# Optimization experiments

Measured on AMD Instinct MI355X. Metric: run time of the kernel, lower is better.

Reference implementation:

```python
import jax, jax.numpy as jnp
import numpy as np

B, T, D, H, K, TAU, L = 1024, 168, 32, 512, 8, 24, 2


def _cell(Wih, Whh, bih, bhh, x_t, h, c):
    # PyTorch LSTM gate order: i, f, g, o
    gates = x_t @ Wih.T + bih + h @ Whh.T + bhh  # [B, 4H]
    i, f, g, o = jnp.split(gates, 4, axis=-1)
    c = jax.nn.sigmoid(f) * c + jax.nn.sigmoid(i) * jnp.tanh(g)
    h = jax.nn.sigmoid(o) * jnp.tanh(c)
    return h, c


def setup_inputs() -> dict:
    key = jax.random.key(0)
    ks = jax.random.split(key, 22)
    s = 1.0 / np.sqrt(H)

    def u(k, shape):
        return jax.random.uniform(k, shape, jnp.float32, -s, s)

    inp = {"x": jax.random.normal(ks[0], (B, T, D), jnp.float32)}
    # encoder LSTM (layer0 input D, layer1 input H)
    inp["enc_Wih0"] = u(ks[1], (4 * H, D)); inp["enc_Whh0"] = u(ks[2], (4 * H, H))
    inp["enc_bih0"] = u(ks[3], (4 * H,));  inp["enc_bhh0"] = u(ks[4], (4 * H,))
    inp["enc_Wih1"] = u(ks[5], (4 * H, H)); inp["enc_Whh1"] = u(ks[6], (4 * H, H))
    inp["enc_bih1"] = u(ks[7], (4 * H,));  inp["enc_bhh1"] = u(ks[8], (4 * H,))
    # decoder LSTM (both layers input H since d_enopt == d_model)
    inp["dec_Wih0"] = u(ks[9], (4 * H, H));  inp["dec_Whh0"] = u(ks[10], (4 * H, H))
    inp["dec_bih0"] = u(ks[11], (4 * H,));   inp["dec_bhh0"] = u(ks[12], (4 * H,))
    inp["dec_Wih1"] = u(ks[13], (4 * H, H)); inp["dec_Whh1"] = u(ks[14], (4 * H, H))
    inp["dec_bih1"] = u(ks[15], (4 * H,));   inp["dec_bhh1"] = u(ks[16], (4 * H,))
    # output heads
    inp["W1"] = u(ks[17], (K, H)); inp["b1"] = u(ks[18], (K,))
    inp["W2"] = u(ks[19], (K, H)); inp["b2"] = u(ks[20], (K,))
    return inp


def reference(x, enc_Wih0, enc_Whh0, enc_bih0, enc_bhh0,
              enc_Wih1, enc_Whh1, enc_bih1, enc_bhh1,
              dec_Wih0, dec_Whh0, dec_bih0, dec_bhh0,
              dec_Wih1, dec_Whh1, dec_bih1, dec_bhh1,
              W1, b1, W2, b2):
    enc_params = [(enc_Wih0, enc_Whh0, enc_bih0, enc_bhh0),
                  (enc_Wih1, enc_Whh1, enc_bih1, enc_bhh1)]
    dec_params = [(dec_Wih0, dec_Whh0, dec_bih0, dec_bhh0),
                  (dec_Wih1, dec_Whh1, dec_bih1, dec_bhh1)]
    b = x.shape[0]
    h0 = jnp.zeros((L, b, H), x.dtype)
    c0 = jnp.zeros((L, b, H), x.dtype)

    def enc_step(carry, x_t):
        h, c = carry
        inp = x_t
        hs, cs = [], []
        for l, p in enumerate(enc_params):
            hn, cn = _cell(*p, inp, h[l], c[l])
            hs.append(hn); cs.append(cn); inp = hn
        return (jnp.stack(hs), jnp.stack(cs)), None

    (h, c), _ = jax.lax.scan(enc_step, (h0, c0), jnp.swapaxes(x, 0, 1))

    def dec_step(carry, _):
        h, c = carry
        inp = h[L - 1]  # feed top-layer hidden back as input
        hs, cs = [], []
        for l, p in enumerate(dec_params):
            hn, cn = _cell(*p, inp, h[l], c[l])
            hs.append(hn); cs.append(cn); inp = hn
        return (jnp.stack(hs), jnp.stack(cs)), inp  # top-layer output

    _, outs = jax.lax.scan(dec_step, (h, c), None, length=TAU)  # [TAU, B, H]
    out = jnp.swapaxes(outs, 0, 1)  # [B, TAU, H]
    mu = out @ W1.T + b1
    beta = 2.0
    sigma = jax.nn.softplus(beta * (out @ W2.T + b2)) / beta
    return mu, sigma
```

## Files before the change

### kernel.cpp

```cpp
#include <hip/hip_runtime.h>
#include <math.h>

typedef _Float16 f16;
typedef __attribute__((ext_vector_type(8))) _Float16 f16x8;
typedef __attribute__((ext_vector_type(4))) _Float16 f16x4;
typedef __attribute__((ext_vector_type(4))) float f32x4;

namespace {
constexpr int B_ = 1024, T_ = 168, H_ = 512, K_ = 8, TAU_ = 24, U_ = 192;
}

__device__ __forceinline__ float sig_(float x) { return 1.0f / (1.0f + expf(-x)); }

template<int AUX>
__device__ __forceinline__ void gl16(const f16* g, char* l) {
    __builtin_amdgcn_global_load_lds((const __attribute__((address_space(1))) void*)g,
                                     (__attribute__((address_space(3))) void*)l, 16, 0, AUX);
}
__device__ __forceinline__ void st_h_sc1(f16* p, f16 v) {
    unsigned int u = (unsigned int)__builtin_bit_cast(unsigned short, v);
    asm volatile("global_store_short %0, %1, off sc1" :: "v"(p), "v"(u) : "memory");
}
#define MFMA16 __builtin_amdgcn_mfma_f32_16x16x32_f16

struct PP {
    const f16 *xp, *w0p, *wsW;
    const float* bsum;
    const f16* hzero;
    f16 *h0r, *h1r;
    f16* h1dec;
    int *cnt0, *cnt1;
};

extern "C" __global__ void __launch_bounds__(256, 1)
lstm_persist(PP P)
{
    extern __shared__ char lds[];
    const int tid = threadIdx.x;
    const int id2 = (blockIdx.x & 7) * 32 + (blockIdx.x >> 3);
    const int rt  = id2 & 15;
    const int row0 = rt * 64;
    const int j0   = (id2 >> 4) * 32;

    const int lane = tid & 63, wid = tid >> 6;
    const int l16 = lane & 15, lq = lane >> 4;
    const int wr = wid >> 1, wc = wid & 1;
    const int sr = tid >> 3, sl = tid & 7;
    const long ksw = (long)((sl ^ (sr & 7)) << 3);

    long wgrow[4];
    #pragma unroll
    for (int q = 0; q < 4; ++q) {
        const int r = sr + 32 * q;
        wgrow[q] = (long)(((r >> 4) & 3) * H_ + j0 + ((r >> 6) << 4) + (r & 15));
    }
    const int swz = (l16 & 7) << 4;
    const int ab0 = (wr * 32 + l16) * 128;
    const int ab1 = ab0 + 2048;
    int wb[4];
    #pragma unroll
    for (int nf = 0; nf < 4; ++nf) wb[nf] = (wc * 64 + nf * 16 + l16) * 128;

    const size_t WM  = (size_t)2048 * 512;
    const long   NBH = (long)B_ * H_;
    bool dead = false;

    auto waitf = [&](const int* p) {
        if (tid == 0 && !dead) {
            int tries = 0;
            while (__hip_atomic_load(p, __ATOMIC_RELAXED,
                                     __HIP_MEMORY_SCOPE_AGENT) < 16) {
                __builtin_amdgcn_s_sleep(1);
                if (++tries > (1 << 16)) { dead = true; break; }
            }
        }
        __syncthreads();
    };
    auto signal = [&](int* p) {
        asm volatile("s_waitcnt vmcnt(0)" ::: "memory");
        __syncthreads();
        if (tid == 0)
            __hip_atomic_fetch_add(p, 1, __ATOMIC_RELAXED, __HIP_MEMORY_SCOPE_AGENT);
    };

    auto runCell = [&](const f16* Ain, long ldaIn, int ncIn, long KwIn,
                       const f16* Wih, const f16* Hin, const f16* Whh,
                       const float* bs, float* cst, f16* hout) {
        const long aA0 = (long)(row0 + sr) * ldaIn + ksw;
        const long aA1 = aA0 + 32 * ldaIn;
        const long aH0 = (long)(row0 + sr) * H_ + ksw;
        const long aH1 = aH0 + 32 * H_;
        const long wI0 = wgrow[0] * KwIn + ksw, wI1 = wgrow[1] * KwIn + ksw;
        const long wI2 = wgrow[2] * KwIn + ksw, wI3 = wgrow[3] * KwIn + ksw;
        const long wH0 = wgrow[0] * H_ + ksw, wH1 = wgrow[1] * H_ + ksw;
        const long wH2 = wgrow[2] * H_ + ksw, wH3 = wgrow[3] * H_ + ksw;
        const int NC = ncIn + 8;

        auto stageChunk = [&](int ci, int buf) {
            char* lb = lds + buf * 24576;
            if (ci < ncIn) {
                const long k0 = (long)ci << 6;
                gl16<16>(Ain + aA0 + k0, lb + tid * 16);
                gl16<16>(Ain + aA1 + k0, lb + 4096 + tid * 16);
                gl16<0>(Wih + wI0 + k0, lb + 8192  + tid * 16);
                gl16<0>(Wih + wI1 + k0, lb + 12288 + tid * 16);
                gl16<0>(Wih + wI2 + k0, lb + 16384 + tid * 16);
                gl16<0>(Wih + wI3 + k0, lb + 20480 + tid * 16);
            } else {
                const long k0 = (long)(ci - ncIn) << 6;
                gl16<16>(Hin + aH0 + k0, lb + tid * 16);
                gl16<16>(Hin + aH1 + k0, lb + 4096 + tid * 16);
                gl16<0>(Whh + wH0 + k0, lb + 8192  + tid * 16);
                gl16<0>(Whh + wH1 + k0, lb + 12288 + tid * 16);
                gl16<0>(Whh + wH2 + k0, lb + 16384 + tid * 16);
                gl16<0>(Whh + wH3 + k0, lb + 20480 + tid * 16);
            }
        };

        f32x4 acc[4][2];
        #pragma unroll
        for (int nf = 0; nf < 4; ++nf)
            #pragma unroll
            for (int m = 0; m < 2; ++m)
                #pragma unroll
                for (int q = 0; q < 4; ++q) acc[nf][m][q] = 0.f;

        stageChunk(0, 0); stageChunk(1, 1); stageChunk(2, 2);
        stageChunk(3, 3); stageChunk(4, 4);
        int cb = 0, sb = 5;
        for (int i = 0; i < NC; ++i) {
            const int ahead = (NC - 1 - i) < 4 ? (NC - 1 - i) : 4;
            if      (ahead == 4) asm volatile("s_waitcnt vmcnt(24)" ::: "memory");
            else if (ahead == 3) asm volatile("s_waitcnt vmcnt(18)" ::: "memory");
            else if (ahead == 2) asm volatile("s_waitcnt vmcnt(12)" ::: "memory");
            else if (ahead == 1) asm volatile("s_waitcnt vmcnt(6)"  ::: "memory");
            else                 asm volatile("s_waitcnt vmcnt(0)"  ::: "memory");
            __builtin_amdgcn_s_barrier();

            char* lb = lds + cb * 24576;
            #pragma unroll
            for (int ks = 0; ks < 2; ++ks) {
                const int kb = ((ks * 64) + lq * 16) ^ swz;
                f16x8 ah0 = *(const f16x8*)(lb + ab0 + kb);
                f16x8 ah1 = *(const f16x8*)(lb + ab1 + kb);
                #pragma unroll
                for (int nf = 0; nf < 4; ++nf) {
                    f16x8 wv = *(const f16x8*)(lb + 8192 + wb[nf] + kb);
                    acc[nf][0] = MFMA16(ah0, wv, acc[nf][0], 0, 0, 0);
                    acc[nf][1] = MFMA16(ah1, wv, acc[nf][1], 0, 0, 0);
                }
            }
            asm volatile("s_waitcnt lgkmcnt(0)" ::: "memory");
            __builtin_amdgcn_s_barrier();
            if (i + 5 < NC) { stageChunk(i + 5, sb); sb = (sb == 5) ? 0 : sb + 1; }
            cb = (cb == 5) ? 0 : cb + 1;
        }

        const int j = j0 + wc * 16 + l16;
        const float bg0 = bs[j], bg1 = bs[H_ + j];
        const float bg2 = bs[2 * H_ + j], bg3 = bs[3 * H_ + j];
        #pragma unroll
        for (int m = 0; m < 2; ++m)
            #pragma unroll
            for (int r = 0; r < 4; ++r) {
                const int ci = m * 4 + r;
                const int bb = row0 + wr * 32 + m * 16 + lq * 4 + r;
                const long base = (long)bb * H_ + j;
                const float pi = acc[0][m][r] + bg0;
                const float pf = acc[1][m][r] + bg1;
                const float pg = acc[2][m][r] + bg2;
                const float po = acc[3][m][r] + bg3;
                const float cn = sig_(pf) * cst[ci] + sig_(pi) * tanhf(pg);
                const float hn = sig_(po) * tanhf(cn);
                cst[ci] = cn;
                st_h_sc1(&hout[base], (f16)hn);
            }
    };

    float c0st[8], c1st[8];
    #pragma unroll
    for (int i = 0; i < 8; ++i) { c0st[i] = 0.f; c1st[i] = 0.f; }

    for (int u = 0; u < U_; ++u) {
        const bool dec = (u >= T_);
        const f16* h0prev = (u == 0) ? P.hzero : P.h0r + (long)((u - 1) & 7) * NBH;
        const f16* h1prev = (u == 0) ? P.hzero
                          : (u <= T_ ? P.h1r + (long)((u - 1) & 7) * NBH
                                     : P.h1dec + (long)(u - 1 - T_) * NBH);
        f16* h0out = P.h0r + (long)(u & 7) * NBH;

        if (dec) {
            waitf(P.cnt1 + (u - 1) * 16 + rt);
            runCell(h1prev, H_, 8, H_, P.wsW + 3 * WM, h0prev,
                    P.wsW + 4 * WM, P.bsum + 4096, c0st, h0out);
        } else {
            runCell(P.xp + (long)u * B_ * 64, 64, 1, 64, P.w0p, h0prev,
                    P.wsW, P.bsum, c0st, h0out);
        }
        signal(P.cnt0 + u * 16 + rt);

        waitf(P.cnt0 + u * 16 + rt);
        f16* h1out = (u < T_) ? P.h1r + (long)(u & 7) * NBH
                              : P.h1dec + (long)(u - T_) * NBH;
        runCell(h0out, H_, 8, H_,
                dec ? P.wsW + 5 * WM : P.wsW + 1 * WM, h1prev,
                dec ? P.wsW + 6 * WM : P.wsW + 2 * WM,
                P.bsum + (dec ? 6144 : 2048), c1st, h1out);
        signal(P.cnt1 + u * 16 + rt);
    }
}

extern "C" __global__ void __launch_bounds__(256)
padx_kernel(const float* __restrict__ x, f16* __restrict__ xp)
{
    const int idx = blockIdx.x * 256 + threadIdx.x;
    const int t = idx >> 10, b = idx & 1023;
    const float* src = x + ((long)b * T_ + t) * 32;
    f16* dst = xp + (long)idx * 64;
    #pragma unroll
    for (int q = 0; q < 8; ++q) {
        float4 v = *(const float4*)&src[q * 4];
        *(f16x4*)&dst[q * 4] = (f16x4){(f16)v.x, (f16)v.y, (f16)v.z, (f16)v.w};
    }
    #pragma unroll
    for (int q = 8; q < 16; ++q) *(f16x4*)&dst[q * 4] = (f16x4){0, 0, 0, 0};
}

extern "C" __global__ void __launch_bounds__(256)
padw_kernel(const float* __restrict__ w, f16* __restrict__ dst)
{
    const int idx = blockIdx.x * 256 + threadIdx.x;
    const int row = idx >> 4, k4 = idx & 15;
    f16x4 hv = (f16x4){0, 0, 0, 0};
    if (k4 < 8) {
        float4 v = *(const float4*)&w[(long)row * 32 + k4 * 4];
        hv = (f16x4){(f16)v.x, (f16)v.y, (f16)v.z, (f16)v.w};
    }
    *(f16x4*)&dst[(long)row * 64 + k4 * 4] = hv;
}

extern "C" __global__ void __launch_bounds__(256)
wcvt_kernel(const float* s0, const float* s1, const float* s2, const float* s3,
            const float* s4, const float* s5, const float* s6, f16* dst)
{
    const int i = blockIdx.x * 256 + threadIdx.x;
    if (i >= 7 * 262144) return;
    const int m = i >> 18, off = i & 262143;
    const float* s = m == 0 ? s0 : m == 1 ? s1 : m == 2 ? s2 : m == 3 ? s3
                   : m == 4 ? s4 : m == 5 ? s5 : s6;
    float4 v = ((const float4*)s)[off];
    *(f16x4*)&dst[(long)m * 1048576 + (long)off * 4] =
        (f16x4){(f16)v.x, (f16)v.y, (f16)v.z, (f16)v.w};
}

extern "C" __global__ void __launch_bounds__(256)
bias_kernel(const float* a0, const float* b0, const float* a1, const float* b1,
            const float* a2, const float* b2, const float* a3, const float* b3,
            float* out)
{
    const int i = blockIdx.x * 256 + threadIdx.x;
    const int l = i >> 11, k = i & 2047;
    const float* pa = l == 0 ? a0 : l == 1 ? a1 : l == 2 ? a2 : a3;
    const float* pb = l == 0 ? b0 : l == 1 ? b1 : l == 2 ? b2 : b3;
    out[i] = pa[k] + pb[k];
}

extern "C" __global__ void __launch_bounds__(256)
zero16(uint4* p, int n)
{
    for (int i = blockIdx.x * 256 + threadIdx.x; i < n; i += gridDim.x * 256)
        p[i] = make_uint4(0, 0, 0, 0);
}

extern "C" __global__ void __launch_bounds__(256)
head_all(const f16* __restrict__ h1dec,
         const float* __restrict__ W1, const float* __restrict__ b1,
         const float* __restrict__ W2, const float* __restrict__ b2,
         float* __restrict__ out)
{
    const int blk = blockIdx.x;
    const int s = blk >> 6;
    const int idx = (blk & 63) * 256 + threadIdx.x;
    const int b = idx >> 4, rr = idx & 15, k = rr & 7, which = rr >> 3;
    const float* w  = (which ? W2 : W1) + (long)k * H_;
    const f16*   hp = h1dec + ((long)s * B_ + b) * H_;
    float sum = 0.f;
    for (int d = 0; d < H_; d += 8) {
        f16x8  hv = *(const f16x8*)&hp[d];
        float4 w0 = *(const float4*)&w[d];
        float4 w1 = *(const float4*)&w[d + 4];
        sum = fmaf((float)hv[0], w0.x, sum);
        sum = fmaf((float)hv[1], w0.y, sum);
        sum = fmaf((float)hv[2], w0.z, sum);
        sum = fmaf((float)hv[3], w0.w, sum);
        sum = fmaf((float)hv[4], w1.x, sum);
        sum = fmaf((float)hv[5], w1.y, sum);
        sum = fmaf((float)hv[6], w1.z, sum);
        sum = fmaf((float)hv[7], w1.w, sum);
    }
    const long o = ((long)b * TAU_ + s) * K_ + k;
    if (which == 0) {
        out[o] = sum + b1[k];
    } else {
        float z  = 2.0f * (sum + b2[k]);
        float sp = fmaxf(z, 0.0f) + log1pf(expf(-fabsf(z)));
        out[(long)B_ * TAU_ * K_ + o] = 0.5f * sp;
    }
}

extern "C" void kernel_launch(void* const* d_in, const int* in_sizes, int n_in,
                              void* d_out, int out_size, void* d_ws, size_t ws_size,
                              hipStream_t stream)
{
    (void)in_sizes; (void)n_in; (void)out_size; (void)ws_size;

    const float* x     = (const float*)d_in[0];
    const float* eWih0 = (const float*)d_in[1];
    const float* eWhh0 = (const float*)d_in[2];
    const float* ebih0 = (const float*)d_in[3];
    const float* ebhh0 = (const float*)d_in[4];
    const float* eWih1 = (const float*)d_in[5];
    const float* eWhh1 = (const float*)d_in[6];
    const float* ebih1 = (const float*)d_in[7];
    const float* ebhh1 = (const float*)d_in[8];
    const float* dWih0 = (const float*)d_in[9];
    const float* dWhh0 = (const float*)d_in[10];
    const float* dbih0 = (const float*)d_in[11];
    const float* dbhh0 = (const float*)d_in[12];
    const float* dWih1 = (const float*)d_in[13];
    const float* dWhh1 = (const float*)d_in[14];
    const float* dbih1 = (const float*)d_in[15];
    const float* dbhh1 = (const float*)d_in[16];
    const float* W1    = (const float*)d_in[17];
    const float* b1    = (const float*)d_in[18];
    const float* W2    = (const float*)d_in[19];
    const float* b2    = (const float*)d_in[20];
    float* out = (float*)d_out;

    (void)hipFuncSetAttribute((const void*)lstm_persist,
                              hipFuncAttributeMaxDynamicSharedMemorySize, 147456);

    char* wsp = (char*)d_ws;
    auto take = [&](size_t n) { void* p = (void*)wsp; wsp += n; return p; };

    f16* xp    = (f16*)take((size_t)T_ * B_ * 64 * 2);
    f16* w0p   = (f16*)take((size_t)2048 * 64 * 2);
    f16* wsW   = (f16*)take((size_t)7 * 2048 * 512 * 2);
    float* bsum = (float*)take((size_t)4 * 2048 * 4);
    f16* h1dec = (f16*)take((size_t)TAU_ * B_ * H_ * 2);
    f16* h0r   = (f16*)take((size_t)8 * B_ * H_ * 2);
    f16* h1r   = (f16*)take((size_t)8 * B_ * H_ * 2);

    char* zstart = wsp;
    int* cnt0  = (int*)take((size_t)U_ * 16 * 4);
    int* cnt1  = (int*)take((size_t)U_ * 16 * 4);
    f16* hzero = (f16*)take((size_t)B_ * H_ * 2);
    const size_t zeroBytes = (size_t)(wsp - zstart);

    const dim3 blk(256);

    padx_kernel<<<dim3(T_ * B_ / 256), blk, 0, stream>>>(x, xp);
    padw_kernel<<<dim3(128), blk, 0, stream>>>(eWih0, w0p);
    wcvt_kernel<<<dim3(7168), blk, 0, stream>>>(eWhh0, eWih1, eWhh1, dWih0,
                                                dWhh0, dWih1, dWhh1, wsW);
    bias_kernel<<<dim3(32), blk, 0, stream>>>(ebih0, ebhh0, ebih1, ebhh1,
                                              dbih0, dbhh0, dbih1, dbhh1, bsum);
    zero16<<<dim3(256), blk, 0, stream>>>((uint4*)zstart, (int)(zeroBytes / 16));

    PP args;
    args.xp = xp; args.w0p = w0p; args.wsW = wsW; args.bsum = bsum; args.hzero = hzero;
    args.h0r = h0r; args.h1r = h1r; args.h1dec = h1dec;
    args.cnt0 = cnt0; args.cnt1 = cnt1;

    lstm_persist<<<dim3(256), blk, 147456, stream>>>(args);
    head_all<<<dim3(TAU_ * 64), blk, 0, stream>>>(h1dec, W1, b1, W2, b2, out);
}
```

Before: 5.247 ms.

## Wavefront-fuse encoder layer1 step s-1 with layer0 step s in one pipeline

During the encoder, layer-1 of step s-1 and layer-0 of step s now run inside one staged load/MFMA pipeline that shares the 6 LDS buffers. A single combined signal and wait per step replaces the two cross-block syncs per timestep. This targets the grid-wide synchronisation latency and the pipeline fill and drain at each cell boundary. The decoder keeps the sequential two-sync schedule, and a tail call finishes the last layer-1 step. It also issues the next stage before waiting, with prefetch depth 5, and drops the special cache hint on the x input loads. The cost is more complex dependency reasoning and an extra accumulator set, which adds register pressure.

```diff
diff --git a/kernel.cpp b/kernel.cpp
--- a/kernel.cpp
+++ b/kernel.cpp
@@ -64,6 +64,16 @@
     const size_t WM  = (size_t)2048 * 512;
     const long   NBH = (long)B_ * H_;
     bool dead = false;
+
+    struct Cd {
+        const f16 *Ain; long lda; int ncIn; long Kw;
+        const f16 *Wih, *Hin, *Whh;
+        const float* bg; float* cst; f16* hout; bool axc;
+    };
+
+    float c0st[8], c1st[8];
+    #pragma unroll
+    for (int i = 0; i < 8; ++i) { c0st[i] = 0.f; c1st[i] = 0.f; }
 
     auto waitf = [&](const int* p) {
         if (tid == 0 && !dead) {
@@ -76,89 +86,40 @@
         }
         __syncthreads();
     };
-    auto signal = [&](int* p) {
+    auto sig1 = [&](int* p) {
         asm volatile("s_waitcnt vmcnt(0)" ::: "memory");
         __syncthreads();
         if (tid == 0)
             __hip_atomic_fetch_add(p, 1, __ATOMIC_RELAXED, __HIP_MEMORY_SCOPE_AGENT);
     };
-
-    auto runCell = [&](const f16* Ain, long ldaIn, int ncIn, long KwIn,
-                       const f16* Wih, const f16* Hin, const f16* Whh,
-                       const float* bs, float* cst, f16* hout) {
-        const long aA0 = (long)(row0 + sr) * ldaIn + ksw;
-        const long aA1 = aA0 + 32 * ldaIn;
-        const long aH0 = (long)(row0 + sr) * H_ + ksw;
-        const long aH1 = aH0 + 32 * H_;
-        const long wI0 = wgrow[0] * KwIn + ksw, wI1 = wgrow[1] * KwIn + ksw;
-        const long wI2 = wgrow[2] * KwIn + ksw, wI3 = wgrow[3] * KwIn + ksw;
-        const long wH0 = wgrow[0] * H_ + ksw, wH1 = wgrow[1] * H_ + ksw;
-        const long wH2 = wgrow[2] * H_ + ksw, wH3 = wgrow[3] * H_ + ksw;
-        const int NC = ncIn + 8;
-
-        auto stageChunk = [&](int ci, int buf) {
-            char* lb = lds + buf * 24576;
-            if (ci < ncIn) {
-                const long k0 = (long)ci << 6;
-                gl16<16>(Ain + aA0 + k0, lb + tid * 16);
-                gl16<16>(Ain + aA1 + k0, lb + 4096 + tid * 16);
-                gl16<0>(Wih + wI0 + k0, lb + 8192  + tid * 16);
-                gl16<0>(Wih + wI1 + k0, lb + 12288 + tid * 16);
-                gl16<0>(Wih + wI2 + k0, lb + 16384 + tid * 16);
-                gl16<0>(Wih + wI3 + k0, lb + 20480 + tid * 16);
-            } else {
-                const long k0 = (long)(ci - ncIn) << 6;
-                gl16<16>(Hin + aH0 + k0, lb + tid * 16);
-                gl16<16>(Hin + aH1 + k0, lb + 4096 + tid * 16);
-                gl16<0>(Whh + wH0 + k0, lb + 8192  + tid * 16);
-                gl16<0>(Whh + wH1 + k0, lb + 12288 + tid * 16);
-                gl16<0>(Whh + wH2 + k0, lb + 16384 + tid * 16);
-                gl16<0>(Whh + wH3 + k0, lb + 20480 + tid * 16);
+    auto sig2 = [&](int* p, int* q) {
+        asm volatile("s_waitcnt vmcnt(0)" ::: "memory");
+        __syncthreads();
+        if (tid == 0) {
+            __hip_atomic_fetch_add(p, 1, __ATOMIC_RELAXED, __HIP_MEMORY_SCOPE_AGENT);
+            __hip_atomic_fetch_add(q, 1, __ATOMIC_RELAXED, __HIP_MEMORY_SCOPE_AGENT);
+        }
+    };
+
+    auto computeChunk = [&](char* lb, f32x4 (&acc)[4][2]) {
+        #pragma unroll
+        for (int ks = 0; ks < 2; ++ks) {
+            const int kb = ((ks * 64) + lq * 16) ^ swz;
+            f16x8 ah0 = *(const f16x8*)(lb + ab0 + kb);
+            f16x8 ah1 = *(const f16x8*)(lb + ab1 + kb);
+            #pragma unroll
+            for (int nf = 0; nf < 4; ++nf) {
+                f16x8 wv = *(const f16x8*)(lb + 8192 + wb[nf] + kb);
+                acc[nf][0] = MFMA16(ah0, wv, acc[nf][0], 0, 0, 0);
+                acc[nf][1] = MFMA16(ah1, wv, acc[nf][1], 0, 0, 0);
             }
-        };
-
-        f32x4 acc[4][2];
-        #pragma unroll
-        for (int nf = 0; nf < 4; ++nf)
-            #pragma unroll
-            for (int m = 0; m < 2; ++m)
-                #pragma unroll
-                for (int q = 0; q < 4; ++q) acc[nf][m][q] = 0.f;
-
-        stageChunk(0, 0); stageChunk(1, 1); stageChunk(2, 2);
-        stageChunk(3, 3); stageChunk(4, 4);
-        int cb = 0, sb = 5;
-        for (int i = 0; i < NC; ++i) {
-            const int ahead = (NC - 1 - i) < 4 ? (NC - 1 - i) : 4;
-            if      (ahead == 4) asm volatile("s_waitcnt vmcnt(24)" ::: "memory");
-            else if (ahead == 3) asm volatile("s_waitcnt vmcnt(18)" ::: "memory");
-            else if (ahead == 2) asm volatile("s_waitcnt vmcnt(12)" ::: "memory");
-            else if (ahead == 1) asm volatile("s_waitcnt vmcnt(6)"  ::: "memory");
-            else                 asm volatile("s_waitcnt vmcnt(0)"  ::: "memory");
-            __builtin_amdgcn_s_barrier();
-
-            char* lb = lds + cb * 24576;
-            #pragma unroll
-            for (int ks = 0; ks < 2; ++ks) {
-                const int kb = ((ks * 64) + lq * 16) ^ swz;
-                f16x8 ah0 = *(const f16x8*)(lb + ab0 + kb);
-                f16x8 ah1 = *(const f16x8*)(lb + ab1 + kb);
-                #pragma unroll
-                for (int nf = 0; nf < 4; ++nf) {
-                    f16x8 wv = *(const f16x8*)(lb + 8192 + wb[nf] + kb);
-                    acc[nf][0] = MFMA16(ah0, wv, acc[nf][0], 0, 0, 0);
-                    acc[nf][1] = MFMA16(ah1, wv, acc[nf][1], 0, 0, 0);
-                }
-            }
-            asm volatile("s_waitcnt lgkmcnt(0)" ::: "memory");
-            __builtin_amdgcn_s_barrier();
-            if (i + 5 < NC) { stageChunk(i + 5, sb); sb = (sb == 5) ? 0 : sb + 1; }
-            cb = (cb == 5) ? 0 : cb + 1;
         }
-
+    };
+
+    auto epi = [&](const Cd& c, f32x4 (&a)[4][2]) {
         const int j = j0 + wc * 16 + l16;
-        const float bg0 = bs[j], bg1 = bs[H_ + j];
-        const float bg2 = bs[2 * H_ + j], bg3 = bs[3 * H_ + j];
+        const float bg0 = c.bg[j], bg1 = c.bg[H_ + j];
+        const float bg2 = c.bg[2 * H_ + j], bg3 = c.bg[3 * H_ + j];
         #pragma unroll
         for (int m = 0; m < 2; ++m)
             #pragma unroll
@@ -166,47 +127,133 @@
                 const int ci = m * 4 + r;
                 const int bb = row0 + wr * 32 + m * 16 + lq * 4 + r;
                 const long base = (long)bb * H_ + j;
-                const float pi = acc[0][m][r] + bg0;
-                const float pf = acc[1][m][r] + bg1;
-                const float pg = acc[2][m][r] + bg2;
-                const float po = acc[3][m][r] + bg3;
-                const float cn = sig_(pf) * cst[ci] + sig_(pi) * tanhf(pg);
+                const float pi = a[0][m][r] + bg0;
+                const float pf = a[1][m][r] + bg1;
+                const float pg = a[2][m][r] + bg2;
+                const float po = a[3][m][r] + bg3;
+                const float cn = sig_(pf) * c.cst[ci] + sig_(pi) * tanhf(pg);
                 const float hn = sig_(po) * tanhf(cn);
-                cst[ci] = cn;
-                st_h_sc1(&hout[base], (f16)hn);
+                c.cst[ci] = cn;
+                st_h_sc1(&c.hout[base], (f16)hn);
             }
     };
 
-    float c0st[8], c1st[8];
-    #pragma unroll
-    for (int i = 0; i < 8; ++i) { c0st[i] = 0.f; c1st[i] = 0.f; }
-
-    for (int u = 0; u < U_; ++u) {
-        const bool dec = (u >= T_);
-        const f16* h0prev = (u == 0) ? P.hzero : P.h0r + (long)((u - 1) & 7) * NBH;
-        const f16* h1prev = (u == 0) ? P.hzero
-                          : (u <= T_ ? P.h1r + (long)((u - 1) & 7) * NBH
-                                     : P.h1dec + (long)(u - 1 - T_) * NBH);
-        f16* h0out = P.h0r + (long)(u & 7) * NBH;
-
+    auto runPipe = [&](const Cd& c1, const Cd& c0, bool two) {
+        const int NC1 = c1.ncIn + 8;
+        const int NT  = two ? NC1 + c0.ncIn + 8 : NC1;
+
+        auto stageG = [&](int g) {
+            const Cd& c = (g < NC1) ? c1 : c0;
+            const int ci = (g < NC1) ? g : g - NC1;
+            char* lb = lds + (g % 6) * 24576;
+            const f16 *Ap, *Wp; long lda, Kw, k0; bool axc;
+            if (ci < c.ncIn) { Ap = c.Ain; Wp = c.Wih; lda = c.lda; Kw = c.Kw;
+                               k0 = (long)ci << 6; axc = c.axc; }
+            else             { Ap = c.Hin; Wp = c.Whh; lda = H_; Kw = H_;
+                               k0 = (long)(ci - c.ncIn) << 6; axc = false; }
+            const long aB = (long)(row0 + sr) * lda + ksw + k0;
+            if (axc) {
+                gl16<0>(Ap + aB, lb + tid * 16);
+                gl16<0>(Ap + aB + 32 * lda, lb + 4096 + tid * 16);
+            } else {
+                gl16<16>(Ap + aB, lb + tid * 16);
+                gl16<16>(Ap + aB + 32 * lda, lb + 4096 + tid * 16);
+            }
+            #pragma unroll
+            for (int q = 0; q < 4; ++q)
+                gl16<0>(Wp + wgrow[q] * Kw + ksw + k0,
+                        lb + 8192 + q * 4096 + tid * 16);
+        };
+
+        f32x4 acc1[4][2], acc0[4][2];
+        #pragma unroll
+        for (int nf = 0; nf < 4; ++nf)
+            #pragma unroll
+            for (int m = 0; m < 2; ++m)
+                #pragma unroll
+                for (int q = 0; q < 4; ++q) { acc1[nf][m][q] = 0.f; acc0[nf][m][q] = 0.f; }
+
+        stageG(0); stageG(1); stageG(2); stageG(3); stageG(4);
+        for (int i = 0; i < NT; ++i) {
+            if (i + 5 < NT) stageG(i + 5);
+            const int ahead = (NT - 1 - i) < 5 ? (NT - 1 - i) : 5;
+            switch (ahead) {
+                case 5: asm volatile("s_waitcnt vmcnt(30)" ::: "memory"); break;
+                case 4: asm volatile("s_waitcnt vmcnt(24)" ::: "memory"); break;
+                case 3: asm volatile("s_waitcnt vmcnt(18)" ::: "memory"); break;
+                case 2: asm volatile("s_waitcnt vmcnt(12)" ::: "memory"); break;
+                case 1: asm volatile("s_waitcnt vmcnt(6)"  ::: "memory"); break;
+                default: asm volatile("s_waitcnt vmcnt(0)" ::: "memory"); break;
+            }
+            __builtin_amdgcn_s_barrier();
+            char* lb = lds + (i % 6) * 24576;
+            if (i < NC1) computeChunk(lb, acc1);
+            else         computeChunk(lb, acc0);
+            asm volatile("s_waitcnt lgkmcnt(0)" ::: "memory");
+            __builtin_amdgcn_s_barrier();
+            if (i == NC1 - 1) epi(c1, acc1);
+        }
+        if (two) epi(c0, acc0);
+    };
+
+    auto mkL1 = [&](int u) {
+        const bool dec = u >= T_;
+        Cd c;
+        c.Ain = P.h0r + (long)(u & 7) * NBH; c.lda = H_; c.ncIn = 8; c.Kw = H_;
+        c.Wih = dec ? P.wsW + 5 * WM : P.wsW + 1 * WM;
+        c.Hin = (u == 0) ? P.hzero
+              : (u <= T_ ? P.h1r + (long)((u - 1) & 7) * NBH
+                         : P.h1dec + (long)(u - 1 - T_) * NBH);
+        c.Whh = dec ? P.wsW + 6 * WM : P.wsW + 2 * WM;
+        c.bg = P.bsum + (dec ? 6144 : 2048); c.cst = c1st;
+        c.hout = (u < T_) ? P.h1r + (long)(u & 7) * NBH
+                          : P.h1dec + (long)(u - T_) * NBH;
+        c.axc = false;
+        return c;
+    };
+    auto mkL0 = [&](int u) {
+        const bool dec = u >= T_;
+        Cd c;
         if (dec) {
-            waitf(P.cnt1 + (u - 1) * 16 + rt);
-            runCell(h1prev, H_, 8, H_, P.wsW + 3 * WM, h0prev,
-                    P.wsW + 4 * WM, P.bsum + 4096, c0st, h0out);
+            c.Ain = (u - 1 < T_) ? P.h1r + (long)((u - 1) & 7) * NBH
+                                 : P.h1dec + (long)(u - 1 - T_) * NBH;
+            c.lda = H_; c.ncIn = 8; c.Kw = H_; c.Wih = P.wsW + 3 * WM; c.axc = false;
         } else {
-            runCell(P.xp + (long)u * B_ * 64, 64, 1, 64, P.w0p, h0prev,
-                    P.wsW, P.bsum, c0st, h0out);
+            c.Ain = P.xp + (long)u * B_ * 64;
+            c.lda = 64; c.ncIn = 1; c.Kw = 64; c.Wih = P.w0p; c.axc = true;
         }
-        signal(P.cnt0 + u * 16 + rt);
-
-        waitf(P.cnt0 + u * 16 + rt);
-        f16* h1out = (u < T_) ? P.h1r + (long)(u & 7) * NBH
-                              : P.h1dec + (long)(u - T_) * NBH;
-        runCell(h0out, H_, 8, H_,
-                dec ? P.wsW + 5 * WM : P.wsW + 1 * WM, h1prev,
-                dec ? P.wsW + 6 * WM : P.wsW + 2 * WM,
-                P.bsum + (dec ? 6144 : 2048), c1st, h1out);
-        signal(P.cnt1 + u * 16 + rt);
+        c.Hin = (u == 0) ? P.hzero : P.h0r + (long)((u - 1) & 7) * NBH;
+        c.Whh = dec ? P.wsW + 4 * WM : P.wsW;
+        c.bg = P.bsum + (dec ? 4096 : 0); c.cst = c0st;
+        c.hout = P.h0r + (long)(u & 7) * NBH;
+        return c;
+    };
+
+    { Cd c = mkL0(0); runPipe(c, c, false); sig1(P.cnt0 + 0 * 16 + rt); }
+
+    for (int s = 1; s < T_; ++s) {
+        waitf(P.cnt0 + (s - 1) * 16 + rt);
+        Cd c1 = mkL1(s - 1);
+        Cd c0 = mkL0(s);
+        runPipe(c1, c0, true);
+        sig2(P.cnt1 + (s - 1) * 16 + rt, P.cnt0 + s * 16 + rt);
+    }
+
+    for (int s = T_; s < U_; ++s) {
+        waitf(P.cnt0 + (s - 1) * 16 + rt);
+        Cd c1 = mkL1(s - 1);
+        runPipe(c1, c1, false);
+        sig1(P.cnt1 + (s - 1) * 16 + rt);
+        waitf(P.cnt1 + (s - 1) * 16 + rt);
+        Cd c0 = mkL0(s);
+        runPipe(c0, c0, false);
+        sig1(P.cnt0 + s * 16 + rt);
+    }
+
+    {
+        waitf(P.cnt0 + (U_ - 1) * 16 + rt);
+        Cd c1 = mkL1(U_ - 1);
+        runPipe(c1, c1, false);
     }
 }
 
```

Result: slower. 6.511 ms (+24.1%).

## Split LSTM layers into two concurrent persistent block chains

Applied to the files above, without the earlier changes.

Launches twice as many persistent blocks, two per CU, and assigns layer 0 and layer 1 to separate block chains. Layer 1 of step u can then run while layer 0 of step u+1 proceeds, instead of each block doing both layers in sequence. Layer 0 waits on layer 1 only up to an 8-deep ring-buffer lag, plus the feedback dependency in the decoder. To fit two blocks per CU, the LDS pipeline shrinks from 6 to 3 stages (prefetch depth 5 to 3), which risks exposing more load latency. It also doubles the number of spin-waiting blocks.

```diff
diff --git a/kernel.cpp b/kernel.cpp
--- a/kernel.cpp
+++ b/kernel.cpp
@@ -32,15 +32,19 @@
     int *cnt0, *cnt1;
 };
 
-extern "C" __global__ void __launch_bounds__(256, 1)
+extern "C" __global__ void __launch_bounds__(256, 2)
 lstm_persist(PP P)
 {
     extern __shared__ char lds[];
     const int tid = threadIdx.x;
-    const int id2 = (blockIdx.x & 7) * 32 + (blockIdx.x >> 3);
-    const int rt  = id2 & 15;
+    const int id2 = (blockIdx.x & 7) * 64 + (blockIdx.x >> 3);
+    const int wv  = id2 & 63;
+    const int chain = wv & 1;
+    const int tt  = wv >> 1;
+    const int rt  = tt & 15;
+    const int jt  = (id2 >> 6) * 2 + (tt >> 4);
     const int row0 = rt * 64;
-    const int j0   = (id2 >> 4) * 32;
+    const int j0   = jt * 32;
 
     const int lane = tid & 63, wid = tid >> 6;
     const int l16 = lane & 15, lq = lane >> 4;
@@ -48,18 +52,20 @@
     const int sr = tid >> 3, sl = tid & 7;
     const long ksw = (long)((sl ^ (sr & 7)) << 3);
 
-    long wgrow[4];
-    #pragma unroll
-    for (int q = 0; q < 4; ++q) {
+    auto wgf = [&](int q) {
         const int r = sr + 32 * q;
-        wgrow[q] = (long)(((r >> 4) & 3) * H_ + j0 + ((r >> 6) << 4) + (r & 15));
-    }
+        return (long)(((r >> 4) & 3) * H_ + j0 + ((r >> 6) << 4) + (r & 15));
+    };
+    const long wgr0 = wgf(0), wgr1 = wgf(1), wgr2 = wgf(2), wgr3 = wgf(3);
+    const long wgH0 = wgr0 * H_ + ksw, wgH1 = wgr1 * H_ + ksw;
+    const long wgH2 = wgr2 * H_ + ksw, wgH3 = wgr3 * H_ + ksw;
+    const long aH0k = (long)(row0 + sr) * H_ + ksw, aH1k = aH0k + 32 * H_;
+
     const int swz = (l16 & 7) << 4;
     const int ab0 = (wr * 32 + l16) * 128;
     const int ab1 = ab0 + 2048;
-    int wb[4];
-    #pragma unroll
-    for (int nf = 0; nf < 4; ++nf) wb[nf] = (wc * 64 + nf * 16 + l16) * 128;
+    const int wb0 = (wc * 64 + 0 * 16 + l16) * 128, wb1 = (wc * 64 + 1 * 16 + l16) * 128;
+    const int wb2 = (wc * 64 + 2 * 16 + l16) * 128, wb3 = (wc * 64 + 3 * 16 + l16) * 128;
 
     const size_t WM  = (size_t)2048 * 512;
     const long   NBH = (long)B_ * H_;
@@ -76,47 +82,81 @@
         }
         __syncthreads();
     };
-    auto signal = [&](int* p) {
+    auto sig1 = [&](int* p) {
         asm volatile("s_waitcnt vmcnt(0)" ::: "memory");
         __syncthreads();
         if (tid == 0)
             __hip_atomic_fetch_add(p, 1, __ATOMIC_RELAXED, __HIP_MEMORY_SCOPE_AGENT);
     };
 
-    auto runCell = [&](const f16* Ain, long ldaIn, int ncIn, long KwIn,
+    auto computeChunk = [&](char* lb, f32x4 (&acc)[4][2]) {
+        #pragma unroll
+        for (int ks = 0; ks < 2; ++ks) {
+            const int kb = ((ks * 64) + lq * 16) ^ swz;
+            f16x8 ah0 = *(const f16x8*)(lb + ab0 + kb);
+            f16x8 ah1 = *(const f16x8*)(lb + ab1 + kb);
+            f16x8 w0 = *(const f16x8*)(lb + 8192 + wb0 + kb);
+            f16x8 w1 = *(const f16x8*)(lb + 8192 + wb1 + kb);
+            f16x8 w2 = *(const f16x8*)(lb + 8192 + wb2 + kb);
+            f16x8 w3 = *(const f16x8*)(lb + 8192 + wb3 + kb);
+            acc[0][0] = MFMA16(ah0, w0, acc[0][0], 0, 0, 0);
+            acc[0][1] = MFMA16(ah1, w0, acc[0][1], 0, 0, 0);
+            acc[1][0] = MFMA16(ah0, w1, acc[1][0], 0, 0, 0);
+            acc[1][1] = MFMA16(ah1, w1, acc[1][1], 0, 0, 0);
+            acc[2][0] = MFMA16(ah0, w2, acc[2][0], 0, 0, 0);
+            acc[2][1] = MFMA16(ah1, w2, acc[2][1], 0, 0, 0);
+            acc[3][0] = MFMA16(ah0, w3, acc[3][0], 0, 0, 0);
+            acc[3][1] = MFMA16(ah1, w3, acc[3][1], 0, 0, 0);
+        }
+    };
+
+    auto epiF = [&](const float* bg, float* cst, f16* hout, f32x4 (&a)[4][2]) {
+        const int j = j0 + wc * 16 + l16;
+        const float bg0 = bg[j], bg1 = bg[H_ + j];
+        const float bg2 = bg[2 * H_ + j], bg3 = bg[3 * H_ + j];
+        #pragma unroll
+        for (int m = 0; m < 2; ++m)
+            #pragma unroll
+            for (int r = 0; r < 4; ++r) {
+                const int ci = m * 4 + r;
+                const int bb = row0 + wr * 32 + m * 16 + lq * 4 + r;
+                const long base = (long)bb * H_ + j;
+                const float pi = a[0][m][r] + bg0;
+                const float pf = a[1][m][r] + bg1;
+                const float pg = a[2][m][r] + bg2;
+                const float po = a[3][m][r] + bg3;
+                const float cn = sig_(pf) * cst[ci] + sig_(pi) * tanhf(pg);
+                const float hn = sig_(po) * tanhf(cn);
+                cst[ci] = cn;
+                st_h_sc1(&hout[base], (f16)hn);
+            }
+    };
+
+    float cst[8];
+    #pragma unroll
+    for (int i = 0; i < 8; ++i) cst[i] = 0.f;
+
+    auto runCell = [&](const f16* Ain, long lda, int ncIn, long Kw,
                        const f16* Wih, const f16* Hin, const f16* Whh,
-                       const float* bs, float* cst, f16* hout) {
-        const long aA0 = (long)(row0 + sr) * ldaIn + ksw;
-        const long aA1 = aA0 + 32 * ldaIn;
-        const long aH0 = (long)(row0 + sr) * H_ + ksw;
-        const long aH1 = aH0 + 32 * H_;
-        const long wI0 = wgrow[0] * KwIn + ksw, wI1 = wgrow[1] * KwIn + ksw;
-        const long wI2 = wgrow[2] * KwIn + ksw, wI3 = wgrow[3] * KwIn + ksw;
-        const long wH0 = wgrow[0] * H_ + ksw, wH1 = wgrow[1] * H_ + ksw;
-        const long wH2 = wgrow[2] * H_ + ksw, wH3 = wgrow[3] * H_ + ksw;
+                       const float* bg, f16* hout) {
+        const long aA0 = (long)(row0 + sr) * lda + ksw;
+        const long aA1 = aA0 + 32 * lda;
+        const long wK0 = wgr0 * Kw + ksw, wK1 = wgr1 * Kw + ksw;
+        const long wK2 = wgr2 * Kw + ksw, wK3 = wgr3 * Kw + ksw;
         const int NC = ncIn + 8;
-
-        auto stageChunk = [&](int ci, int buf) {
-            char* lb = lds + buf * 24576;
-            if (ci < ncIn) {
-                const long k0 = (long)ci << 6;
-                gl16<16>(Ain + aA0 + k0, lb + tid * 16);
-                gl16<16>(Ain + aA1 + k0, lb + 4096 + tid * 16);
-                gl16<0>(Wih + wI0 + k0, lb + 8192  + tid * 16);
-                gl16<0>(Wih + wI1 + k0, lb + 12288 + tid * 16);
-                gl16<0>(Wih + wI2 + k0, lb + 16384 + tid * 16);
-                gl16<0>(Wih + wI3 + k0, lb + 20480 + tid * 16);
-            } else {
-                const long k0 = (long)(ci - ncIn) << 6;
-                gl16<16>(Hin + aH0 + k0, lb + tid * 16);
-                gl16<16>(Hin + aH1 + k0, lb + 4096 + tid * 16);
-                gl16<0>(Whh + wH0 + k0, lb + 8192  + tid * 16);
-                gl16<0>(Whh + wH1 + k0, lb + 12288 + tid * 16);
-                gl16<0>(Whh + wH2 + k0, lb + 16384 + tid * 16);
-                gl16<0>(Whh + wH3 + k0, lb + 20480 + tid * 16);
-            }
+        auto st = [&](int ci) {
+            char* lb = lds + (ci % 3) * 24576;
+            const bool inp = ci < ncIn;
+            const long k0 = (long)(inp ? ci : ci - ncIn) << 6;
+            const f16* Ap = inp ? Ain : Hin;
+            const f16* Wp = inp ? Wih : Whh;
+            gl16<16>(Ap + (inp ? aA0 : aH0k) + k0, lb + tid * 16);
+            gl16<16>(Ap + (inp ? aA1 : aH1k) + k0, lb + 4096 + tid * 16);
+            gl16<0>(Wp + (inp ? wK0 : wgH0) + k0, lb + 8192  + tid * 16);
+            gl16<0>(Wp + (inp ? wK1 : wgH1) + k0, lb + 12288 + tid * 16);
+            gl16<0>(Wp + (inp ? wK2 : wgH2) + k0, lb + 16384 + tid * 16);
+            gl16<0>(Wp + (inp ? wK3 : wgH3) + k0, lb + 20480 + tid * 16);
         };
-
         f32x4 acc[4][2];
         #pragma unroll
         for (int nf = 0; nf < 4; ++nf)
@@ -124,89 +164,56 @@
             for (int m = 0; m < 2; ++m)
                 #pragma unroll
                 for (int q = 0; q < 4; ++q) acc[nf][m][q] = 0.f;
-
-        stageChunk(0, 0); stageChunk(1, 1); stageChunk(2, 2);
-        stageChunk(3, 3); stageChunk(4, 4);
-        int cb = 0, sb = 5;
+        st(0); st(1); st(2);
         for (int i = 0; i < NC; ++i) {
-            const int ahead = (NC - 1 - i) < 4 ? (NC - 1 - i) : 4;
-            if      (ahead == 4) asm volatile("s_waitcnt vmcnt(24)" ::: "memory");
-            else if (ahead == 3) asm volatile("s_waitcnt vmcnt(18)" ::: "memory");
-            else if (ahead == 2) asm volatile("s_waitcnt vmcnt(12)" ::: "memory");
+            const int ahead = (NC - 1 - i) < 2 ? (NC - 1 - i) : 2;
+            if      (ahead == 2) asm volatile("s_waitcnt vmcnt(12)" ::: "memory");
             else if (ahead == 1) asm volatile("s_waitcnt vmcnt(6)"  ::: "memory");
             else                 asm volatile("s_waitcnt vmcnt(0)"  ::: "memory");
             __builtin_amdgcn_s_barrier();
-
-            char* lb = lds + cb * 24576;
-            #pragma unroll
-            for (int ks = 0; ks < 2; ++ks) {
-                const int kb = ((ks * 64) + lq * 16) ^ swz;
-                f16x8 ah0 = *(const f16x8*)(lb + ab0 + kb);
-                f16x8 ah1 = *(const f16x8*)(lb + ab1 + kb);
-                #pragma unroll
-                for (int nf = 0; nf < 4; ++nf) {
-                    f16x8 wv = *(const f16x8*)(lb + 8192 + wb[nf] + kb);
-                    acc[nf][0] = MFMA16(ah0, wv, acc[nf][0], 0, 0, 0);
-                    acc[nf][1] = MFMA16(ah1, wv, acc[nf][1], 0, 0, 0);
-                }
-            }
+            computeChunk(lds + (i % 3) * 24576, acc);
             asm volatile("s_waitcnt lgkmcnt(0)" ::: "memory");
             __builtin_amdgcn_s_barrier();
-            if (i + 5 < NC) { stageChunk(i + 5, sb); sb = (sb == 5) ? 0 : sb + 1; }
-            cb = (cb == 5) ? 0 : cb + 1;
-        }
-
-        const int j = j0 + wc * 16 + l16;
-        const float bg0 = bs[j], bg1 = bs[H_ + j];
-        const float bg2 = bs[2 * H_ + j], bg3 = bs[3 * H_ + j];
-        #pragma unroll
-        for (int m = 0; m < 2; ++m)
-            #pragma unroll
-            for (int r = 0; r < 4; ++r) {
-                const int ci = m * 4 + r;
-                const int bb = row0 + wr * 32 + m * 16 + lq * 4 + r;
-                const long base = (long)bb * H_ + j;
-                const float pi = acc[0][m][r] + bg0;
-                const float pf = acc[1][m][r] + bg1;
-                const float pg = acc[2][m][r] + bg2;
-                const float po = acc[3][m][r] + bg3;
-                const float cn = sig_(pf) * cst[ci] + sig_(pi) * tanhf(pg);
-                const float hn = sig_(po) * tanhf(cn);
-                cst[ci] = cn;
-                st_h_sc1(&hout[base], (f16)hn);
+            if (i + 3 < NC) st(i + 3);
+        }
+        epiF(bg, cst, hout, acc);
+    };
+
+    if (chain == 0) {
+        for (int u = 0; u < U_; ++u) {
+            const bool dec = (u >= T_);
+            if (u > 0) waitf(P.cnt0 + (u - 1) * 16 + rt);
+            if (dec)   waitf(P.cnt1 + (u - 1) * 16 + rt);
+            else if (u >= 8) waitf(P.cnt1 + (u - 8) * 16 + rt);
+            const f16* h0prev = (u == 0) ? P.hzero : P.h0r + (long)((u - 1) & 7) * NBH;
+            f16* h0out = P.h0r + (long)(u & 7) * NBH;
+            if (dec) {
+                const f16* h1prev = (u <= T_) ? P.h1r + (long)((u - 1) & 7) * NBH
+                                              : P.h1dec + (long)(u - 1 - T_) * NBH;
+                runCell(h1prev, H_, 8, H_, P.wsW + 3 * WM, h0prev,
+                        P.wsW + 4 * WM, P.bsum + 4096, h0out);
+            } else {
+                runCell(P.xp + (long)u * B_ * 64, 64, 1, 64, P.w0p, h0prev,
+                        P.wsW, P.bsum, h0out);
             }
-    };
-
-    float c0st[8], c1st[8];
-    #pragma unroll
-    for (int i = 0; i < 8; ++i) { c0st[i] = 0.f; c1st[i] = 0.f; }
-
-    for (int u = 0; u < U_; ++u) {
-        const bool dec = (u >= T_);
-        const f16* h0prev = (u == 0) ? P.hzero : P.h0r + (long)((u - 1) & 7) * NBH;
-        const f16* h1prev = (u == 0) ? P.hzero
-                          : (u <= T_ ? P.h1r + (long)((u - 1) & 7) * NBH
-                                     : P.h1dec + (long)(u - 1 - T_) * NBH);
-        f16* h0out = P.h0r + (long)(u & 7) * NBH;
-
-        if (dec) {
-            waitf(P.cnt1 + (u - 1) * 16 + rt);
-            runCell(h1prev, H_, 8, H_, P.wsW + 3 * WM, h0prev,
-                    P.wsW + 4 * WM, P.bsum + 4096, c0st, h0out);
-        } else {
-            runCell(P.xp + (long)u * B_ * 64, 64, 1, 64, P.w0p, h0prev,
-                    P.wsW, P.bsum, c0st, h0out);
-        }
-        signal(P.cnt0 + u * 16 + rt);
-
-        waitf(P.cnt0 + u * 16 + rt);
-        f16* h1out = (u < T_) ? P.h1r + (long)(u & 7) * NBH
-                              : P.h1dec + (long)(u - T_) * NBH;
-        runCell(h0out, H_, 8, H_,
-                dec ? P.wsW + 5 * WM : P.wsW + 1 * WM, h1prev,
-                dec ? P.wsW + 6 * WM : P.wsW + 2 * WM,
-                P.bsum + (dec ? 6144 : 2048), c1st, h1out);
-        signal(P.cnt1 + u * 16 + rt);
+            sig1(P.cnt0 + u * 16 + rt);
+        }
+    } else {
+        for (int u = 0; u < U_; ++u) {
+            const bool dec = (u >= T_);
+            waitf(P.cnt0 + u * 16 + rt);
+            if (u > 0) waitf(P.cnt1 + (u - 1) * 16 + rt);
+            const f16* h1prev = (u == 0) ? P.hzero
+                              : (u <= T_ ? P.h1r + (long)((u - 1) & 7) * NBH
+                                         : P.h1dec + (long)(u - 1 - T_) * NBH);
+            f16* h1out = (u < T_) ? P.h1r + (long)(u & 7) * NBH
+                                  : P.h1dec + (long)(u - T_) * NBH;
+            runCell(P.h0r + (long)(u & 7) * NBH, H_, 8, H_,
+                    dec ? P.wsW + 5 * WM : P.wsW + 1 * WM, h1prev,
+                    dec ? P.wsW + 6 * WM : P.wsW + 2 * WM,
+                    P.bsum + (dec ? 6144 : 2048), h1out);
+            sig1(P.cnt1 + u * 16 + rt);
+        }
     }
 }
 
@@ -338,7 +345,7 @@
     float* out = (float*)d_out;
 
     (void)hipFuncSetAttribute((const void*)lstm_persist,
-                              hipFuncAttributeMaxDynamicSharedMemorySize, 147456);
+                              hipFuncAttributeMaxDynamicSharedMemorySize, 73728);
 
     char* wsp = (char*)d_ws;
     auto take = [&](size_t n) { void* p = (void*)wsp; wsp += n; return p; };
@@ -372,6 +379,6 @@
     args.h0r = h0r; args.h1r = h1r; args.h1dec = h1dec;
     args.cnt0 = cnt0; args.cnt1 = cnt1;
 
-    lstm_persist<<<dim3(256), blk, 147456, stream>>>(args);
+    lstm_persist<<<dim3(512), blk, 73728, stream>>>(args);
     head_all<<<dim3(TAU_ * 64), blk, 0, stream>>>(h1dec, W1, b1, W2, b2, out);
 }
```

Result: slower. 6.114 ms (+16.5%).
